# Performance work log

Measured on AMD Instinct MI355X. Metric: run time of the kernel, lower is better.

The kernel has to match this reference:

```python
import jax, jax.numpy as jnp
import numpy as np
import math

HIDDEN = 1024
Q_SIZE = 1024
KV_SIZE = 1024
OUT_SIZE = 1024
N_HEADS = 16
D_K = HIDDEN // N_HEADS


def setup_inputs() -> dict:
    key = jax.random.key(0)
    ks = jax.random.split(key, 9)
    b, s, t = 8, 2048, 512
    sc = 0.02
    return {
        "hiddens": jax.random.normal(ks[0], (b, s, KV_SIZE), jnp.float32),
        "query_hiddens": jax.random.normal(ks[1], (b, t, Q_SIZE), jnp.float32),
        "mask": jax.random.randint(ks[2], (b, s), 0, 2, jnp.int32),
        "W_q": jax.random.normal(ks[3], (Q_SIZE, HIDDEN), jnp.float32) * sc,
        "b_q": jnp.zeros((HIDDEN,), jnp.float32),
        "W_k": jax.random.normal(ks[4], (KV_SIZE, HIDDEN), jnp.float32) * sc,
        "W_v": jax.random.normal(ks[5], (KV_SIZE, HIDDEN), jnp.float32) * sc,
        "W_o": jax.random.normal(ks[6], (HIDDEN, OUT_SIZE), jnp.float32) * sc,
        "b_o": jnp.zeros((OUT_SIZE,), jnp.float32),
    }


def reference(hiddens, query_hiddens, mask, W_q, b_q, W_k, W_v, W_o, b_o):
    b, t, _ = query_hiddens.shape
    s = hiddens.shape[1]
    # projections (dropout p=0 in eval -> identity)
    Q = (query_hiddens @ W_q + b_q).reshape(b, t, N_HEADS, D_K)
    K = (hiddens @ W_k).reshape(b, s, N_HEADS, D_K)
    V = (hiddens @ W_v).reshape(b, s, N_HEADS, D_K)
    # scores: [b, t, s, h] matching e = (Q*K).sum(-1)/sqrt(d_k)
    e = jnp.einsum('bthd,bshd->btsh', Q, K) / math.sqrt(D_K)
    neg = (1.0 - mask.astype(e.dtype)) * (-1e20)  # [b, s]
    e = e + neg[:, None, :, None]
    a = jax.nn.softmax(e, axis=2)  # softmax over seqlen
    concat = jnp.einsum('btsh,bshd->bthd', a, V).reshape(b, t, HIDDEN)
    context = concat @ W_o + b_o
    return context, a.mean(axis=-1)
```

## Files before the change

### kernel.cpp

```cpp
#include <hip/hip_runtime.h>
#include <hip/hip_bf16.h>

using short8 = __attribute__((ext_vector_type(8))) short;
using f32x4  = __attribute__((ext_vector_type(4))) float;

#define LSK 72

#define GLDS(gptr, lptr) __builtin_amdgcn_global_load_lds( \
    (const __attribute__((address_space(1))) void*)(gptr), \
    (__attribute__((address_space(3))) void*)(lptr), 16, 0, 0)

static __device__ __forceinline__ short f2b(float f) {
    unsigned u = __builtin_bit_cast(unsigned, f);
    unsigned r = (u + 0x7fffu + ((u >> 16) & 1u)) >> 16;
    return (short)r;
}

__global__ void cvt_bf16(const float* __restrict__ in, short* __restrict__ out, int n) {
    int i = (blockIdx.x * 256 + threadIdx.x) * 4;
    if (i >= n) return;
    float4 v = *(const float4*)(in + i);
    short4 o = make_short4(f2b(v.x), f2b(v.y), f2b(v.z), f2b(v.w));
    *(short4*)(out + i) = o;
}

__global__ void cvt_t4(const float* __restrict__ W0, const float* __restrict__ W1,
                       const float* __restrict__ W2, const float* __restrict__ W3,
                       short* __restrict__ Wt0) {
    __shared__ short tile[32][33];
    const float* Ws[4] = {W0, W1, W2, W3};
    const float* W = Ws[blockIdx.z];
    short* Wt = Wt0 + (size_t)blockIdx.z * 1024 * 1024;
    const int K = 1024, N = 1024;
    int n0 = blockIdx.x * 32, k0 = blockIdx.y * 32;
    int tx = threadIdx.x, ty = threadIdx.y;
#pragma unroll
    for (int i = 0; i < 4; i++) {
        int r = ty + i * 8;
        tile[r][tx] = f2b(W[(size_t)(k0 + r) * N + n0 + tx]);
    }
    __syncthreads();
#pragma unroll
    for (int i = 0; i < 4; i++) {
        int r = ty + i * 8;
        Wt[(size_t)(n0 + r) * K + k0 + tx] = tile[tx][r];
    }
}

__global__ __launch_bounds__(256) void gemm128(
    const short* __restrict__ A, const short* __restrict__ Bt,
    const float* __restrict__ bias, void* __restrict__ Cout, void* __restrict__ Cout2,
    int M, int mode)
{
    __shared__ short As[2][128 * 64];
    __shared__ short Bs[2][128 * 64];
    const int tid = threadIdx.x;
    const int w = tid >> 6, L = tid & 63, quad = L >> 4, l16 = L & 15;
    const int wr = w >> 1, wc = w & 1;

    const int lin = blockIdx.y * gridDim.x + blockIdx.x;
    const int xcd = lin & 7, idx = lin >> 3;
    const int mPer = gridDim.y >> 3;
    const int my = xcd * mPer + idx / gridDim.x;
    const int nx = idx % gridDim.x;
    const int n0 = nx * 128, m0 = my * 128;

    const int K = 1024;
    const int srow_in = L >> 3;
    const int sgcol   = ((L & 7) ^ (srow_in & 7)) * 8;

    auto STAGE = [&](int buf, int k0) {
#pragma unroll
        for (int j = 0; j < 8; j++) {
            int c = w * 8 + j;
            if (c < 16) {
                int row = c * 8 + srow_in;
                GLDS(A + (size_t)(m0 + row) * K + k0 + sgcol, &As[buf][c * 512]);
            } else {
                int row = (c - 16) * 8 + srow_in;
                GLDS(Bt + (size_t)(n0 + row) * K + k0 + sgcol, &Bs[buf][(c - 16) * 512]);
            }
        }
    };

    f32x4 acc[4][4];
#pragma unroll
    for (int mi = 0; mi < 4; mi++)
#pragma unroll
        for (int ni = 0; ni < 4; ni++) acc[mi][ni] = (f32x4){0.f, 0.f, 0.f, 0.f};

    STAGE(0, 0);
    __syncthreads();

    for (int t = 0; t < 16; t++) {
        const int cur = t & 1;
        if (t < 15) STAGE(cur ^ 1, (t + 1) * 64);
#pragma unroll
        for (int kk = 0; kk < 64; kk += 32) {
            const int swz = (((kk >> 3) + quad) ^ (l16 & 7)) << 3;
            short8 af[4], bf[4];
#pragma unroll
            for (int mi = 0; mi < 4; mi++)
                af[mi] = *(const short8*)&As[cur][(wr * 64 + mi * 16 + l16) * 64 + swz];
#pragma unroll
            for (int ni = 0; ni < 4; ni++)
                bf[ni] = *(const short8*)&Bs[cur][(wc * 64 + ni * 16 + l16) * 64 + swz];
#pragma unroll
            for (int mi = 0; mi < 4; mi++)
#pragma unroll
                for (int ni = 0; ni < 4; ni++)
                    acc[mi][ni] = __builtin_amdgcn_mfma_f32_16x16x32_bf16(af[mi], bf[ni], acc[mi][ni], 0, 0, 0);
        }
        __syncthreads();
    }

#pragma unroll
    for (int ni = 0; ni < 4; ni++) {
        int n = n0 + wc * 64 + ni * 16 + l16;
        float bv = (mode != 2 && bias) ? bias[n] : 0.f;
#pragma unroll
        for (int mi = 0; mi < 4; mi++) {
#pragma unroll
            for (int r = 0; r < 4; r++) {
                int m = m0 + wr * 64 + mi * 16 + quad * 4 + r;
                float v = acc[mi][ni][r] + bv;
                if (mode == 1)      ((float*)Cout)[(size_t)m * 1024 + n] = v;
                else if (mode == 0) ((short*)Cout)[(size_t)m * 1024 + n] = f2b(v);
                else {
                    if (n < 1024) ((short*)Cout)[(size_t)m * 1024 + n] = f2b(v);
                    else {
                        int h = (n - 1024) >> 6, d = n & 63;
                        int b = m >> 11, s = m & 2047;
                        ((short*)Cout2)[(((size_t)b * 16 + h) * 64 + d) * 2048 + s] = f2b(v);
                    }
                }
            }
        }
    }
}

__global__ __launch_bounds__(512) void attn_flash(
    const short* __restrict__ Qb, const short* __restrict__ Kb, const short* __restrict__ Vtb,
    const int* __restrict__ mask, short* __restrict__ Cb, float* __restrict__ lse)
{
    __shared__ short Qs[128 * 64];
    __shared__ short Ks[2][128 * 64];
    __shared__ short Vts[2][128 * 64];
    __shared__ short Ps[128 * LSK];
    __shared__ float neg[2][128];
    const int tid = threadIdx.x;
    const int w = tid >> 6, L = tid & 63, quad = L >> 4, l16 = L & 15;
    const int t0 = blockIdx.x * 128, h = blockIdx.y, b = blockIdx.z;
    const int S = 2048, T = 512, H = 1024;
    const int trow = w * 16;
    const int srow = L >> 3;
    const int sg   = ((L & 7) ^ srow) * 8;

    auto STAGE_KV = [&](int buf, int s0) {
#pragma unroll
        for (int j = 0; j < 2; j++) {
            int krow = w * 16 + j * 8 + srow;
            GLDS(Kb + ((size_t)b * S + s0 + krow) * H + h * 64 + sg, &Ks[buf][(w * 16 + j * 8) * 64]);
            int c = w * 2 + j, hf = c >> 3, d0 = (c & 7) * 8;
            GLDS(Vtb + (((size_t)b * 16 + h) * 64 + d0 + srow) * S + s0 + hf * 64 + sg, &Vts[buf][c * 512]);
        }
        if (tid < 128) neg[buf][tid] = mask[(size_t)b * S + s0 + tid] ? 0.f : -1e20f;
    };

#pragma unroll
    for (int j = 0; j < 2; j++) {
        int row = w * 16 + j * 8 + srow;
        GLDS(Qb + ((size_t)b * T + t0 + row) * H + h * 64 + sg, &Qs[(w * 16 + j * 8) * 64]);
    }
    STAGE_KV(0, 0);
    __syncthreads();

    short8 aq[2];
#pragma unroll
    for (int kk = 0; kk < 2; kk++)
        aq[kk] = *(const short8*)&Qs[(trow + l16) * 64 + ((kk * 4 + quad) ^ (l16 & 7)) * 8];

    f32x4 Oacc[4];
#pragma unroll
    for (int nt = 0; nt < 4; nt++) Oacc[nt] = (f32x4){0.f, 0.f, 0.f, 0.f};
    float lsum[4] = {0.f, 0.f, 0.f, 0.f};

    for (int it = 0; it < 16; it++) {
        const int cur = it & 1;
        if (it < 15) STAGE_KV(cur ^ 1, (it + 1) * 128);
#pragma unroll
        for (int hf = 0; hf < 2; hf++) {
            f32x4 sacc[4];
#pragma unroll
            for (int nt = 0; nt < 4; nt++) sacc[nt] = (f32x4){0.f, 0.f, 0.f, 0.f};
#pragma unroll
            for (int kk = 0; kk < 2; kk++) {
#pragma unroll
                for (int nt = 0; nt < 4; nt++) {
                    short8 bf = *(const short8*)&Ks[cur][(hf * 64 + nt * 16 + l16) * 64 + ((kk * 4 + quad) ^ (l16 & 7)) * 8];
                    sacc[nt] = __builtin_amdgcn_mfma_f32_16x16x32_bf16(aq[kk], bf, sacc[nt], 0, 0, 0);
                }
            }
#pragma unroll
            for (int nt = 0; nt < 4; nt++) {
                float ng = neg[cur][hf * 64 + nt * 16 + l16];
#pragma unroll
                for (int r = 0; r < 4; r++) {
                    float e = __expf(fmaf(sacc[nt][r], 0.125f, ng));
                    lsum[r] += e;
                    Ps[(trow + quad * 4 + r) * LSK + nt * 16 + l16] = f2b(e);
                }
            }
#pragma unroll
            for (int kk = 0; kk < 2; kk++) {
                short8 af = *(const short8*)&Ps[(trow + l16) * LSK + kk * 32 + quad * 8];
#pragma unroll
                for (int nt = 0; nt < 4; nt++) {
                    short8 bf = *(const short8*)&Vts[cur][hf * 4096 + (nt * 16 + l16) * 64 + ((kk * 4 + quad) ^ (l16 & 7)) * 8];
                    Oacc[nt] = __builtin_amdgcn_mfma_f32_16x16x32_bf16(af, bf, Oacc[nt], 0, 0, 0);
                }
            }
        }
        __syncthreads();
    }
#pragma unroll
    for (int r = 0; r < 4; r++) {
#pragma unroll
        for (int off = 1; off < 16; off <<= 1)
            lsum[r] += __shfl_xor(lsum[r], off, 64);
    }
#pragma unroll
    for (int r = 0; r < 4; r++) {
        float inv = 1.0f / lsum[r];
        int t = t0 + trow + quad * 4 + r;
#pragma unroll
        for (int nt = 0; nt < 4; nt++) {
            int d = nt * 16 + l16;
            Cb[((size_t)b * T + t) * H + h * 64 + d] = f2b(Oacc[nt][r] * inv);
        }
        if (l16 == 0)
            lse[((size_t)b * 16 + h) * T + t] = __logf(lsum[r]);
    }
}

__global__ __launch_bounds__(256) void attn_amean(
    const short* __restrict__ Qb, const short* __restrict__ Kb,
    const int* __restrict__ mask, const float* __restrict__ lse, float* __restrict__ outA)
{
    __shared__ short Qs[2][64 * 64];
    __shared__ short Ks[2][64 * 64];
    __shared__ float neg[64];
    __shared__ float lss[16 * 64];
    const int tid = threadIdx.x;
    const int w = tid >> 6, L = tid & 63, quad = L >> 4, l16 = L & 15;
    const int s0 = blockIdx.x * 64, t0 = blockIdx.y * 64, b = blockIdx.z;
    const int S = 2048, T = 512, H = 1024;
    const int srow = L >> 3;
    const int sg   = ((L & 7) ^ srow) * 8;

    auto STAGE_QK = [&](int buf, int h) {
#pragma unroll
        for (int j = 0; j < 2; j++) {
            int row = w * 16 + j * 8 + srow;
            GLDS(Qb + ((size_t)b * T + t0 + row) * H + h * 64 + sg, &Qs[buf][(w * 16 + j * 8) * 64]);
            GLDS(Kb + ((size_t)b * S + s0 + row) * H + h * 64 + sg, &Ks[buf][(w * 16 + j * 8) * 64]);
        }
    };

    if (tid < 64) neg[tid] = mask[(size_t)b * S + s0 + tid] ? 0.f : -1e20f;
    for (int i = tid; i < 16 * 64; i += 256) {
        int hh = i >> 6, tt = i & 63;
        lss[i] = lse[((size_t)b * 16 + hh) * T + t0 + tt];
    }
    STAGE_QK(0, 0);
    __syncthreads();

    float am[4][4] = {};
    for (int h = 0; h < 16; h++) {
        const int cur = h & 1;
        if (h < 15) STAGE_QK(cur ^ 1, h + 1);
        short8 aq[2];
#pragma unroll
        for (int kk = 0; kk < 2; kk++)
            aq[kk] = *(const short8*)&Qs[cur][(w * 16 + l16) * 64 + ((kk * 4 + quad) ^ (l16 & 7)) * 8];
        f32x4 sacc[4];
#pragma unroll
        for (int nt = 0; nt < 4; nt++) sacc[nt] = (f32x4){0.f, 0.f, 0.f, 0.f};
#pragma unroll
        for (int kk = 0; kk < 2; kk++) {
#pragma unroll
            for (int nt = 0; nt < 4; nt++) {
                short8 bf = *(const short8*)&Ks[cur][(nt * 16 + l16) * 64 + ((kk * 4 + quad) ^ (l16 & 7)) * 8];
                sacc[nt] = __builtin_amdgcn_mfma_f32_16x16x32_bf16(aq[kk], bf, sacc[nt], 0, 0, 0);
            }
        }
#pragma unroll
        for (int nt = 0; nt < 4; nt++) {
            float ng = neg[nt * 16 + l16];
#pragma unroll
            for (int r = 0; r < 4; r++) {
                int trow = w * 16 + quad * 4 + r;
                am[nt][r] += __expf(fmaf(sacc[nt][r], 0.125f, ng - lss[h * 64 + trow]));
            }
        }
        __syncthreads();
    }
#pragma unroll
    for (int r = 0; r < 4; r++) {
        int t = t0 + w * 16 + quad * 4 + r;
#pragma unroll
        for (int nt = 0; nt < 4; nt++) {
            int s = s0 + nt * 16 + l16;
            outA[((size_t)b * T + t) * S + s] = am[nt][r] * 0.0625f;
        }
    }
}

extern "C" void kernel_launch(void* const* d_in, const int* in_sizes, int n_in,
                              void* d_out, int out_size, void* d_ws, size_t ws_size,
                              hipStream_t stream) {
    const float* hiddens = (const float*)d_in[0];
    const float* query   = (const float*)d_in[1];
    const int*   mask    = (const int*)d_in[2];
    const float* W_q = (const float*)d_in[3];
    const float* b_q = (const float*)d_in[4];
    const float* W_k = (const float*)d_in[5];
    const float* W_v = (const float*)d_in[6];
    const float* W_o = (const float*)d_in[7];
    const float* b_o = (const float*)d_in[8];
    float* out = (float*)d_out;

    constexpr size_t N_H  = 8UL * 2048 * 1024;
    constexpr size_t N_QH = 8UL * 512 * 1024;
    constexpr size_t N_W  = 1024UL * 1024;
    char* ws = (char*)d_ws;
    short* Hb   = (short*)(ws);
    short* QHb  = (short*)(ws + N_H * 2);
    short* Wqt  = (short*)(ws + N_H * 2 + N_QH * 2);
    short* Wkt  = Wqt + N_W;
    short* Wvt  = Wkt + N_W;
    short* Wot  = Wvt + N_W;
    short* Qb   = Wot + N_W;
    short* Kb   = Qb + N_QH;
    short* Vtb  = Kb + N_H;
    short* Cb   = Vtb + N_H;
    float* lseP = (float*)(Cb + N_QH);

    cvt_bf16<<<16384, 256, 0, stream>>>(hiddens, Hb, (int)N_H);
    cvt_bf16<<<4096, 256, 0, stream>>>(query, QHb, (int)N_QH);
    cvt_t4<<<dim3(32, 32, 4), dim3(32, 8), 0, stream>>>(W_q, W_k, W_v, W_o, Wqt);

    gemm128<<<dim3(8, 32), 256, 0, stream>>>(QHb, Wqt, b_q, Qb, nullptr, 4096, 0);
    gemm128<<<dim3(16, 128), 256, 0, stream>>>(Hb, Wkt, nullptr, Kb, Vtb, 16384, 2);

    attn_flash<<<dim3(4, 16, 8), 512, 0, stream>>>(Qb, Kb, Vtb, mask, Cb, lseP);

    gemm128<<<dim3(8, 32), 256, 0, stream>>>(Cb, Wot, b_o, out, nullptr, 4096, 1);
    attn_amean<<<dim3(32, 8, 8), 256, 0, stream>>>(Qb, Kb, mask, lseP, out + N_QH);
}
```

Baseline: 433.2 us.

## Use 256x256-tile 512-thread GEMM for fused K/V projection

Adds a dedicated gemm256 kernel with 256x256 output tiles, 8 waves, double-buffered global-to-LDS loads staged across four sub-steps, and MFMA priority raising. It replaces the 128x128 gemm128 launch for the large K/V projection (16384x2048x1024). The goal is more data reuse per LDS load and better overlap of loads with compute. In exchange it uses 128 KB of LDS per block with launch bounds requesting 2 blocks per CU, which may limit occupancy. The generic kernel's strided transposed-V store path is removed, and its bias handling is simplified.

```diff
diff --git a/kernel.cpp b/kernel.cpp
--- a/kernel.cpp
+++ b/kernel.cpp
@@ -47,6 +47,104 @@
     }
 }
 
+__global__ __launch_bounds__(512, 2) void gemm256(
+    const short* __restrict__ A, const short* __restrict__ Bt,
+    short* __restrict__ CK, short* __restrict__ CVt)
+{
+    __shared__ short As[2][256 * 64];
+    __shared__ short Bs[2][256 * 64];
+    const int tid = threadIdx.x;
+    const int w = tid >> 6, L = tid & 63, quad = L >> 4, l16 = L & 15;
+    const int wr = w >> 2, wcn = w & 3;
+
+    const int lin = blockIdx.y * gridDim.x + blockIdx.x;
+    const int xcd = lin & 7, idx = lin >> 3;
+    const int mPer = gridDim.y >> 3;
+    const int my = xcd * mPer + idx / gridDim.x;
+    const int nx = idx % gridDim.x;
+    const int n0 = nx * 256, m0 = my * 256;
+
+    const int K = 1024;
+    const int srow_in = L >> 3;
+    const int sgcol   = ((L & 7) ^ srow_in) * 8;
+
+    auto STAGE2 = [&](int buf, int kt, int p) {
+#pragma unroll
+        for (int j = 0; j < 2; j++) {
+            int c = w * 8 + p * 2 + j;
+            int k0 = kt * 64;
+            if (c < 32) {
+                int row = c * 8 + srow_in;
+                GLDS(A + (size_t)(m0 + row) * K + k0 + sgcol, &As[buf][c * 512]);
+            } else {
+                int row = (c - 32) * 8 + srow_in;
+                GLDS(Bt + (size_t)(n0 + row) * K + k0 + sgcol, &Bs[buf][(c - 32) * 512]);
+            }
+        }
+    };
+
+    f32x4 acc[2][4][4];
+#pragma unroll
+    for (int mh = 0; mh < 2; mh++)
+#pragma unroll
+        for (int mi = 0; mi < 4; mi++)
+#pragma unroll
+            for (int ni = 0; ni < 4; ni++) acc[mh][mi][ni] = (f32x4){0.f, 0.f, 0.f, 0.f};
+
+#pragma unroll
+    for (int p = 0; p < 4; p++) STAGE2(0, 0, p);
+
+    for (int t = 0; t < 16; t++) {
+        const int cur = t & 1;
+#pragma unroll
+        for (int p = 0; p < 4; p++) {
+            if (t < 15) STAGE2(cur ^ 1, t + 1, p);
+            if (p == 0) {
+                if (t < 15) asm volatile("s_waitcnt vmcnt(2)" ::: "memory");
+                else        asm volatile("s_waitcnt vmcnt(0)" ::: "memory");
+                __builtin_amdgcn_s_barrier();
+            }
+            const int mh = p & 1, kk = (p >> 1) * 32;
+            const int swz = (((kk >> 3) + quad) ^ (l16 & 7)) << 3;
+            short8 af[4], bf[4];
+#pragma unroll
+            for (int mi = 0; mi < 4; mi++)
+                af[mi] = *(const short8*)&As[cur][(wr * 128 + mh * 64 + mi * 16 + l16) * 64 + swz];
+#pragma unroll
+            for (int ni = 0; ni < 4; ni++)
+                bf[ni] = *(const short8*)&Bs[cur][(wcn * 64 + ni * 16 + l16) * 64 + swz];
+            __builtin_amdgcn_s_setprio(1);
+#pragma unroll
+            for (int mi = 0; mi < 4; mi++)
+#pragma unroll
+                for (int ni = 0; ni < 4; ni++)
+                    acc[mh][mi][ni] = __builtin_amdgcn_mfma_f32_16x16x32_bf16(af[mi], bf[ni], acc[mh][mi][ni], 0, 0, 0);
+            __builtin_amdgcn_s_setprio(0);
+            __builtin_amdgcn_s_barrier();
+        }
+    }
+
+#pragma unroll
+    for (int mh = 0; mh < 2; mh++)
+#pragma unroll
+        for (int ni = 0; ni < 4; ni++) {
+            int n = n0 + wcn * 64 + ni * 16 + l16;
+#pragma unroll
+            for (int mi = 0; mi < 4; mi++)
+#pragma unroll
+                for (int r = 0; r < 4; r++) {
+                    int m = m0 + wr * 128 + mh * 64 + mi * 16 + quad * 4 + r;
+                    float v = acc[mh][mi][ni][r];
+                    if (n < 1024) CK[(size_t)m * 1024 + n] = f2b(v);
+                    else {
+                        int h = (n - 1024) >> 6, d = n & 63;
+                        int b = m >> 11, s = m & 2047;
+                        CVt[(((size_t)b * 16 + h) * 64 + d) * 2048 + s] = f2b(v);
+                    }
+                }
+        }
+}
+
 __global__ __launch_bounds__(256) void gemm128(
     const short* __restrict__ A, const short* __restrict__ Bt,
     const float* __restrict__ bias, void* __restrict__ Cout, void* __restrict__ Cout2,
@@ -117,7 +215,7 @@
 #pragma unroll
     for (int ni = 0; ni < 4; ni++) {
         int n = n0 + wc * 64 + ni * 16 + l16;
-        float bv = (mode != 2 && bias) ? bias[n] : 0.f;
+        float bv = bias ? bias[n] : 0.f;
 #pragma unroll
         for (int mi = 0; mi < 4; mi++) {
 #pragma unroll
@@ -125,15 +223,7 @@
                 int m = m0 + wr * 64 + mi * 16 + quad * 4 + r;
                 float v = acc[mi][ni][r] + bv;
                 if (mode == 1)      ((float*)Cout)[(size_t)m * 1024 + n] = v;
-                else if (mode == 0) ((short*)Cout)[(size_t)m * 1024 + n] = f2b(v);
-                else {
-                    if (n < 1024) ((short*)Cout)[(size_t)m * 1024 + n] = f2b(v);
-                    else {
-                        int h = (n - 1024) >> 6, d = n & 63;
-                        int b = m >> 11, s = m & 2047;
-                        ((short*)Cout2)[(((size_t)b * 16 + h) * 64 + d) * 2048 + s] = f2b(v);
-                    }
-                }
+                else                ((short*)Cout)[(size_t)m * 1024 + n] = f2b(v);
             }
         }
     }
@@ -351,7 +441,7 @@
     cvt_t4<<<dim3(32, 32, 4), dim3(32, 8), 0, stream>>>(W_q, W_k, W_v, W_o, Wqt);
 
     gemm128<<<dim3(8, 32), 256, 0, stream>>>(QHb, Wqt, b_q, Qb, nullptr, 4096, 0);
-    gemm128<<<dim3(16, 128), 256, 0, stream>>>(Hb, Wkt, nullptr, Kb, Vtb, 16384, 2);
+    gemm256<<<dim3(8, 64), 512, 0, stream>>>(Hb, Wkt, Kb, Vtb);
 
     attn_flash<<<dim3(4, 16, 8), 512, 0, stream>>>(Qb, Kb, Vtb, mask, Cb, lseP);
 
```

Result: no change. 433.7 us (+0.1%).
